# Optimization experiments

Hardware: AMD Instinct MI355X
Metric: run time of the kernel (lower is better)

Reference implementation:

```python
import jax, jax.numpy as jnp
import numpy as np

B, T, CIN, HF, G, E = 8, 316, 64, 128, 32, 384
DOWN, MINP, OUT = 2, 8, 8
STRIDE = MINP // DOWN  # finest-grid cell -> feature-map stride


def _build_metas(b, t):
    # Non-overlapping quadtree partition of the 32x32 finest grid:
    # 8x8 macro cells (span 4) all split into span-2 nodes; the first 20 of
    # those are split again into span-1 leaves -> 236 + 80 = 316 tokens.
    # meta row = [tl_row_fg, tl_col_fg, cell_span, patch_px, score]
    span2 = [(r + dr, c + dc) for r in range(0, G, 4) for c in range(0, G, 4)
             for dr in (0, 2) for dc in (0, 2)]
    rows = [[r, c, 2, 16, 0] for (r, c) in span2[20:]]
    rows += [[r + dr, c + dc, 1, 8, 0] for (r, c) in span2[:20]
             for dr in (0, 1) for dc in (0, 1)]
    meta = np.asarray(rows, np.int32)
    rng = np.random.default_rng(0)
    return jnp.asarray(np.stack([meta[rng.permutation(t)] for _ in range(b)], 0))


def setup_inputs():
    key = jax.random.key(0)
    k1, k2 = jax.random.split(key)
    return {
        "x_in": jax.random.normal(k1, (B, CIN, HF, HF), jnp.float32),
        "tokens": jax.random.normal(k2, (B, T, E), jnp.float32),
        "metas": _build_metas(B, T),
    }


def _sample_token(img, r_fg, c_fg, p_px):
    # img: [C, Hf, Wf]. Bilinear resize (align_corners=False, matching
    # F.interpolate) of the [p_feat, p_feat] crop at (r_fg*STRIDE, c_fg*STRIDE)
    # to [OUT, OUT], fully in-place via gathers (no host syncs, no per-token
    # kernel launches).
    p_feat = p_px // DOWN
    pf = jnp.maximum(p_feat, 1).astype(jnp.float32)
    i = jnp.arange(OUT, dtype=jnp.float32)
    rel = jnp.clip((i + 0.5) * (pf / OUT) - 0.5, 0.0, pf - 1.0)
    i0 = jnp.floor(rel)
    w = rel - i0
    i1 = jnp.minimum(i0 + 1.0, pf - 1.0)
    off_r = (r_fg * STRIDE).astype(jnp.float32)
    off_c = (c_fg * STRIDE).astype(jnp.float32)
    y0 = (off_r + i0).astype(jnp.int32); y1 = (off_r + i1).astype(jnp.int32)
    x0 = (off_c + i0).astype(jnp.int32); x1 = (off_c + i1).astype(jnp.int32)
    g = lambda y, x: img[:, y[:, None], x[None, :]]  # [C, OUT, OUT]
    wx = w[None, None, :]; wy = w[None, :, None]
    top = g(y0, x0) * (1 - wx) + g(y0, x1) * wx
    bot = g(y1, x0) * (1 - wx) + g(y1, x1) * wx
    patch = top * (1 - wy) + bot * wy
    return jnp.where(p_px > 0, patch, 0.0)


def _extract_patches(x_in, metas):
    per_img = lambda img, mb: jax.vmap(
        lambda m: _sample_token(img, m[0], m[1], m[3]))(mb)
    return jax.vmap(per_img)(x_in, metas)  # [B, T, C, OUT, OUT]


def _spatial_scatter(tokens, metas):
    # Each token's embedding is tiled over its span x span finest-grid cells.
    # Build an owner-index map via one scatter, then one gather.
    b, t, e = tokens.shape
    r, c, span, p = metas[..., 0], metas[..., 1], metas[..., 2], metas[..., 3]
    di, dj = np.meshgrid(np.arange(4), np.arange(4), indexing="ij")  # max span 4
    di = jnp.asarray(di.reshape(-1)); dj = jnp.asarray(dj.reshape(-1))  # [16]
    rows = r[:, :, None] + di
    cols = c[:, :, None] + dj                                   # [B, T, 16]
    valid = (di < span[:, :, None]) & (dj < span[:, :, None]) & (p[:, :, None] > 0)
    flat = jnp.where(valid, rows * G + cols, G * G)             # dump slot G*G
    owner = jnp.full((b, G * G + 1), -1, jnp.int32)
    b_idx = jnp.arange(b)[:, None, None]
    t_idx = jnp.broadcast_to(jnp.arange(t, dtype=jnp.int32)[None, :, None], flat.shape)
    owner = owner.at[b_idx, flat].set(t_idx)[:, : G * G]        # [B, G*G]
    gathered = jnp.take_along_axis(tokens, jnp.maximum(owner, 0)[:, :, None], axis=1)
    fmap = jnp.where(owner[:, :, None] >= 0, gathered, 0.0)     # [B, G*G, E]
    return fmap.reshape(b, G, G, e).transpose(0, 3, 1, 2)       # [B, E, G, G]


def reference(x_in, tokens, metas):
    patches = _extract_patches(x_in, metas)
    half_span = metas[..., 2].astype(jnp.float32) / 2.0
    cx = metas[..., 1].astype(jnp.float32) + half_span
    cy = metas[..., 0].astype(jnp.float32) + half_span
    p = metas[..., 3]
    scale_idx = jnp.where(p == 16, 1, jnp.where(p == 8, 2, 0)).astype(jnp.int32)
    fmap = _spatial_scatter(tokens, metas)
    return patches, cx, cy, scale_idx, fmap
```

## Files before the change

### kernel.cpp

```cpp
#include <hip/hip_runtime.h>

#define B_      8
#define T_      316
#define CIN_    64
#define HF_     128
#define G_      32
#define E_      384
#define OUT_    8

#define PATCH_SZ  10354688
#define CX_OFF    (PATCH_SZ)
#define CY_OFF    (CX_OFF + B_*T_)
#define SI_OFF    (CY_OFF + B_*T_)
#define FMAP_OFF  (SI_OFF + B_*T_)

#define NBAND_ 16
#define NCHG_  8
#define NP_    (B_ * NBAND_ * NCHG_)

#define EG_    16
#define NF_    (B_ * (E_ / EG_))

#define LDSC_ 1088

#define WS_OWN    0
#define WS_OWN16  (B_ * G_ * G_)
#define WS_P8     (WS_OWN16 + B_ * NBAND_ * 16)

__device__ __forceinline__ void load16(float* d, const float* p)
{
    const float4* q = (const float4*)p;
#pragma unroll
    for (int k = 0; k < 4; ++k) {
        const float4 v = q[k];
        d[4*k+0] = v.x; d[4*k+1] = v.y; d[4*k+2] = v.z; d[4*k+3] = v.w;
    }
}

__global__ __launch_bounds__(192)
void meta_kernel(const int* __restrict__ metas,
                 float* __restrict__ out,
                 int* __restrict__ ws)
{
    const int b    = blockIdx.x >> 1;
    const int half = blockIdx.x & 1;
    if (threadIdx.x >= 158) return;
    const int t = half * 158 + threadIdx.x;

    const int4 m = *(const int4*)(metas + (b * T_ + t) * 5);
    const int r = m.x, c = m.y, s = m.z, p = m.w;

    const float hs = (float)s * 0.5f;
    out[CX_OFF + b * T_ + t] = (float)c + hs;
    out[CY_OFF + b * T_ + t] = (float)r + hs;
    out[SI_OFF + b * T_ + t] = (p == 16) ? 1.0f : ((p == 8) ? 2.0f : 0.0f);

    int* own = ws + WS_OWN + b * (G_ * G_);
    if (p == 16) {
        ws[WS_OWN16 + (b * NBAND_ + (r >> 1)) * 16 + (c >> 1)] = t;
        own[r * G_ + c]           = t;
        own[r * G_ + c + 1]       = t;
        own[(r + 1) * G_ + c]     = t;
        own[(r + 1) * G_ + c + 1] = t;
    } else if (p == 8) {
        ws[WS_P8 + (b * 2 + (r >> 1)) * 40 + (r & 1) * 20 + c] = t;
        own[r * G_ + c] = t;
    }
}

__global__ __launch_bounds__(256)
void fused_kernel(const float* __restrict__ x,
                  const float* __restrict__ tokens,
                  const int* __restrict__ ws,
                  float* __restrict__ out)
{
    const int blk = blockIdx.x;
    const int tid = threadIdx.x;

    if (blk >= NF_) {
        const int pb = blk - NF_;
        int b, gr, chg;
        if (pb < 2 * NCHG_ * B_) {
            b   = pb >> 4;
            gr  = (pb >> 3) & 1;
            chg = pb & 7;
        } else {
            const int q = pb - 2 * NCHG_ * B_;
            b   = q / (14 * NCHG_);
            const int rdm = q % (14 * NCHG_);
            gr  = 2 + (rdm >> 3);
            chg = rdm & 7;
        }

        __shared__ __align__(16) float sm[8 * LDSC_];
        __shared__ int own16b[16];
        __shared__ int p8tok[40];

        if (tid < 16)
            own16b[tid] = ws[WS_OWN16 + (b * NBAND_ + gr) * 16 + tid];
        if (gr < 2 && tid < 40)
            p8tok[tid] = ws[WS_P8 + (b * 2 + gr) * 40 + tid];

        const int row  = tid >> 5;
        const int col4 = tid & 31;
        const int cp   = col4 >> 1;
        const int j4   = col4 & 1;
        const int w    = row * 2 + j4;

        const float* src = x + ((size_t)b * CIN_ + chg * 8) * (HF_ * HF_)
                             + (8 * gr + row) * HF_ + col4 * 4;
        float* dst = sm + cp * 68 + w * 4;
#pragma unroll
        for (int ccl = 0; ccl < 8; ++ccl)
            *(float4*)(dst + ccl * LDSC_) = *(const float4*)(src + (size_t)ccl * (HF_ * HF_));
        __syncthreads();

        {
            const int cpo = tid >> 4;
            const int wo  = tid & 15;
            const int tok = (gr < 2 && cpo < 10) ? -1 : own16b[cpo];
            if (tok >= 0) {
                float4* po4 = (float4*)out + (size_t)(b * T_ + tok) * 1024;
                const float* ls = sm + cpo * 68 + wo * 4;
#pragma unroll
                for (int ccl = 0; ccl < 8; ++ccl)
                    po4[(chg * 8 + ccl) * 16 + wo] = *(const float4*)(ls + ccl * LDSC_);
            }
        }

        if (gr < 2) {
            for (int e0 = 0; e0 < 40; e0 += 2) {
                const int e   = e0 + (tid >> 7);
                const int tk  = p8tok[e];
                const int rl  = (e >= 20) ? 1 : 0;
                const int cc  = e - rl * 20;
                const int u   = tid & 127;
                const int ccl = u >> 4;
                const int ww  = u & 15;
                const int i   = ww >> 1;
                const int j4w = ww & 1;

                const float* cell = sm + ccl * LDSC_ + (cc >> 1) * 68
                                       + (cc & 1) * 4 + 32 * rl;

                const float reli = fminf(fmaxf(((float)i + 0.5f) * 0.5f - 0.5f, 0.0f), 3.0f);
                const float fi0  = floorf(reli);
                const float wy   = reli - fi0;
                const int   y0   = (int)fi0;
                const int   y1   = (int)fminf(fi0 + 1.0f, 3.0f);

                float res[4];
#pragma unroll
                for (int jj = 0; jj < 4; ++jj) {
                    const int j = j4w * 4 + jj;
                    const float relj = fminf(fmaxf(((float)j + 0.5f) * 0.5f - 0.5f, 0.0f), 3.0f);
                    const float fj0  = floorf(relj);
                    const float wx   = relj - fj0;
                    const int   x0   = (int)fj0;
                    const int   x1   = (int)fminf(fj0 + 1.0f, 3.0f);
                    const float t0 = cell[y0 * 8 + x0] * (1.0f - wx) + cell[y0 * 8 + x1] * wx;
                    const float t1 = cell[y1 * 8 + x0] * (1.0f - wx) + cell[y1 * 8 + x1] * wx;
                    res[jj] = t0 * (1.0f - wy) + t1 * wy;
                }
                ((float4*)out)[(size_t)(b * T_ + tk) * 1024 + (chg * 8 + ccl) * 16 + ww] =
                    make_float4(res[0], res[1], res[2], res[3]);
            }
        }
        return;
    }

    const int b  = blk & 7;
    const int eg = blk >> 3;

    const int4 o = ((const int4*)(ws + WS_OWN + b * (G_ * G_)))[tid];
    const float* tok = tokens + (size_t)b * T_ * E_ + eg * EG_;

    float a0[16], a1[16], a2[16], a3[16];
    load16(a0, tok + (size_t)o.x * E_);
    load16(a1, tok + (size_t)o.y * E_);
    load16(a2, tok + (size_t)o.z * E_);
    load16(a3, tok + (size_t)o.w * E_);

    float4* fm = (float4*)(out + FMAP_OFF + (size_t)b * E_ * (G_ * G_)
                                          + (size_t)eg * EG_ * (G_ * G_));
#pragma unroll
    for (int e = 0; e < EG_; ++e) {
        float4 v; v.x = a0[e]; v.y = a1[e]; v.z = a2[e]; v.w = a3[e];
        fm[e * 256 + tid] = v;
    }
}

extern "C" void kernel_launch(void* const* d_in, const int* in_sizes, int n_in,
                              void* d_out, int out_size, void* d_ws, size_t ws_size,
                              hipStream_t stream) {
    const float* x_in   = (const float*)d_in[0];
    const float* tokens = (const float*)d_in[1];
    const int*   metas  = (const int*)d_in[2];
    float*       out    = (float*)d_out;
    int*         ws     = (int*)d_ws;

    meta_kernel<<<2 * B_, 192, 0, stream>>>(metas, out, ws);
    fused_kernel<<<NF_ + NP_, 256, 0, stream>>>(x_in, tokens, ws, out);
}
```

Baseline: 96.69 us.

## Fold meta preprocessing into fused kernel, rebuilding owner maps in shared memory

```diff
diff --git a/kernel.cpp b/kernel.cpp
--- a/kernel.cpp
+++ b/kernel.cpp
@@ -23,10 +23,6 @@
 
 #define LDSC_ 1088
 
-#define WS_OWN    0
-#define WS_OWN16  (B_ * G_ * G_)
-#define WS_P8     (WS_OWN16 + B_ * NBAND_ * 16)
-
 __device__ __forceinline__ void load16(float* d, const float* p)
 {
     const float4* q = (const float4*)p;
@@ -37,41 +33,10 @@
     }
 }
 
-__global__ __launch_bounds__(192)
-void meta_kernel(const int* __restrict__ metas,
-                 float* __restrict__ out,
-                 int* __restrict__ ws)
-{
-    const int b    = blockIdx.x >> 1;
-    const int half = blockIdx.x & 1;
-    if (threadIdx.x >= 158) return;
-    const int t = half * 158 + threadIdx.x;
-
-    const int4 m = *(const int4*)(metas + (b * T_ + t) * 5);
-    const int r = m.x, c = m.y, s = m.z, p = m.w;
-
-    const float hs = (float)s * 0.5f;
-    out[CX_OFF + b * T_ + t] = (float)c + hs;
-    out[CY_OFF + b * T_ + t] = (float)r + hs;
-    out[SI_OFF + b * T_ + t] = (p == 16) ? 1.0f : ((p == 8) ? 2.0f : 0.0f);
-
-    int* own = ws + WS_OWN + b * (G_ * G_);
-    if (p == 16) {
-        ws[WS_OWN16 + (b * NBAND_ + (r >> 1)) * 16 + (c >> 1)] = t;
-        own[r * G_ + c]           = t;
-        own[r * G_ + c + 1]       = t;
-        own[(r + 1) * G_ + c]     = t;
-        own[(r + 1) * G_ + c + 1] = t;
-    } else if (p == 8) {
-        ws[WS_P8 + (b * 2 + (r >> 1)) * 40 + (r & 1) * 20 + c] = t;
-        own[r * G_ + c] = t;
-    }
-}
-
 __global__ __launch_bounds__(256)
 void fused_kernel(const float* __restrict__ x,
                   const float* __restrict__ tokens,
-                  const int* __restrict__ ws,
+                  const int* __restrict__ metas,
                   float* __restrict__ out)
 {
     const int blk = blockIdx.x;
@@ -96,10 +61,13 @@
         __shared__ int own16b[16];
         __shared__ int p8tok[40];
 
-        if (tid < 16)
-            own16b[tid] = ws[WS_OWN16 + (b * NBAND_ + gr) * 16 + tid];
-        if (gr < 2 && tid < 40)
-            p8tok[tid] = ws[WS_P8 + (b * 2 + gr) * 40 + tid];
+        for (int t = tid; t < T_; t += 256) {
+            const int4 m = *(const int4*)(metas + (b * T_ + t) * 5);
+            if ((m.x >> 1) == gr) {
+                if (m.w == 16) own16b[m.y >> 1] = t;
+                else           p8tok[(m.x & 1) * 20 + m.y] = t;
+            }
+        }
 
         const int row  = tid >> 5;
         const int col4 = tid & 31;
@@ -129,37 +97,44 @@
         }
 
         if (gr < 2) {
+            const int u   = tid & 127;
+            const int ccl = u >> 4;
+            const int ww  = u & 15;
+            const int i   = ww >> 1;
+            const int j4w = ww & 1;
+
+            const float reli = fminf(fmaxf(((float)i + 0.5f) * 0.5f - 0.5f, 0.0f), 3.0f);
+            const float fi0  = floorf(reli);
+            const float wy   = reli - fi0;
+            const int   y0   = (int)fi0;
+            const int   y1   = (int)fminf(fi0 + 1.0f, 3.0f);
+            float wx[4]; int x0[4], x1[4];
+#pragma unroll
+            for (int jj = 0; jj < 4; ++jj) {
+                const int j = j4w * 4 + jj;
+                const float relj = fminf(fmaxf(((float)j + 0.5f) * 0.5f - 0.5f, 0.0f), 3.0f);
+                const float fj0  = floorf(relj);
+                wx[jj] = relj - fj0;
+                x0[jj] = (int)fj0;
+                x1[jj] = (int)fminf(fj0 + 1.0f, 3.0f);
+            }
+
             for (int e0 = 0; e0 < 40; e0 += 2) {
                 const int e   = e0 + (tid >> 7);
                 const int tk  = p8tok[e];
                 const int rl  = (e >= 20) ? 1 : 0;
                 const int cc  = e - rl * 20;
-                const int u   = tid & 127;
-                const int ccl = u >> 4;
-                const int ww  = u & 15;
-                const int i   = ww >> 1;
-                const int j4w = ww & 1;
 
                 const float* cell = sm + ccl * LDSC_ + (cc >> 1) * 68
                                        + (cc & 1) * 4 + 32 * rl;
 
-                const float reli = fminf(fmaxf(((float)i + 0.5f) * 0.5f - 0.5f, 0.0f), 3.0f);
-                const float fi0  = floorf(reli);
-                const float wy   = reli - fi0;
-                const int   y0   = (int)fi0;
-                const int   y1   = (int)fminf(fi0 + 1.0f, 3.0f);
-
                 float res[4];
 #pragma unroll
                 for (int jj = 0; jj < 4; ++jj) {
-                    const int j = j4w * 4 + jj;
-                    const float relj = fminf(fmaxf(((float)j + 0.5f) * 0.5f - 0.5f, 0.0f), 3.0f);
-                    const float fj0  = floorf(relj);
-                    const float wx   = relj - fj0;
-                    const int   x0   = (int)fj0;
-                    const int   x1   = (int)fminf(fj0 + 1.0f, 3.0f);
-                    const float t0 = cell[y0 * 8 + x0] * (1.0f - wx) + cell[y0 * 8 + x1] * wx;
-                    const float t1 = cell[y1 * 8 + x0] * (1.0f - wx) + cell[y1 * 8 + x1] * wx;
+                    const float t0 = cell[y0 * 8 + x0[jj]] * (1.0f - wx[jj])
+                                   + cell[y0 * 8 + x1[jj]] * wx[jj];
+                    const float t1 = cell[y1 * 8 + x0[jj]] * (1.0f - wx[jj])
+                                   + cell[y1 * 8 + x1[jj]] * wx[jj];
                     res[jj] = t0 * (1.0f - wy) + t1 * wy;
                 }
                 ((float4*)out)[(size_t)(b * T_ + tk) * 1024 + (chg * 8 + ccl) * 16 + ww] =
@@ -172,7 +147,23 @@
     const int b  = blk & 7;
     const int eg = blk >> 3;
 
-    const int4 o = ((const int4*)(ws + WS_OWN + b * (G_ * G_)))[tid];
+    __shared__ int own[G_ * G_];
+
+    for (int t = tid; t < T_; t += 256) {
+        const int4 m = *(const int4*)(metas + (b * T_ + t) * 5);
+        if (eg == 0) {
+            const float hs = (float)m.z * 0.5f;
+            out[CX_OFF + b * T_ + t] = (float)m.y + hs;
+            out[CY_OFF + b * T_ + t] = (float)m.x + hs;
+            out[SI_OFF + b * T_ + t] = (m.w == 16) ? 1.0f : ((m.w == 8) ? 2.0f : 0.0f);
+        }
+        int* o = own + m.x * G_ + m.y;
+        if (m.w == 16) { o[0] = t; o[1] = t; o[G_] = t; o[G_ + 1] = t; }
+        else           { o[0] = t; }
+    }
+    __syncthreads();
+
+    const int4 o = ((const int4*)own)[tid];
     const float* tok = tokens + (size_t)b * T_ * E_ + eg * EG_;
 
     float a0[16], a1[16], a2[16], a3[16];
@@ -197,8 +188,6 @@
     const float* tokens = (const float*)d_in[1];
     const int*   metas  = (const int*)d_in[2];
     float*       out    = (float*)d_out;
-    int*         ws     = (int*)d_ws;
 
-    meta_kernel<<<2 * B_, 192, 0, stream>>>(metas, out, ws);
-    fused_kernel<<<NF_ + NP_, 256, 0, stream>>>(x_in, tokens, ws, out);
+    fused_kernel<<<NF_ + NP_, 256, 0, stream>>>(x_in, tokens, metas, out);
 }
```

Result: no change. 95.44 us (-1.3%).
